# Performance work log

Measured on AMD Instinct MI355X. Metric: run time of the kernel, lower is better.

The kernel has to match this reference:

```python
import jax, jax.numpy as jnp
import numpy as np

N, H = 8192, 256
TOP_K = 16          # k = min(top_k, N-1)
TEMPERATURE = 1.0
NEG_SLOPE = 0.2
NUM_SECTORS = 11


def setup_inputs() -> dict:
    key = jax.random.key(0)
    kE, kW, ka, ks, kA = jax.random.split(key, 5)
    embeddings = jax.random.normal(kE, (N, H), dtype=jnp.float32)
    # xavier-uniform-like scale for W (nn.Linear, bias=False)
    lim = float(np.sqrt(6.0 / (H + H)))
    W = jax.random.uniform(kW, (H, H), dtype=jnp.float32, minval=-lim, maxval=lim)
    # a ~ Normal(0, 1/sqrt(2H))
    a = jax.random.normal(ka, (2 * H,), dtype=jnp.float32) * (1.0 / np.sqrt(2 * H))
    sector_ids = jax.random.randint(ks, (N,), 0, NUM_SECTORS, dtype=jnp.int32)
    active_mask = jax.random.randint(kA, (N,), 0, 2, dtype=jnp.int32).astype(bool)
    return {"embeddings": embeddings, "W": W, "a": a,
            "sector_ids": sector_ids, "active_mask": active_mask}


def reference(embeddings, W, a, sector_ids, active_mask):
    # h = W(embeddings)  (torch Linear: x @ W.T)
    h = embeddings @ W.T                                   # [N, H]
    # attention[i,j] = leaky_relu(a . [h_i, h_j]) = leaky_relu(a1.h_i + a2.h_j)
    # (decomposition of the concat+matmul; same math, avoids O(N^2*2H) tensor)
    a1, a2 = a[:H], a[H:]
    s_i = h @ a1                                           # [N]
    s_j = h @ a2                                           # [N]
    att = jax.nn.leaky_relu(s_i[:, None] + s_j[None, :], NEG_SLOPE) / TEMPERATURE
    # combined mask: active pairs AND same sector
    mask = (active_mask[:, None] & active_mask[None, :]) \
           & (sector_ids[:, None] == sector_ids[None, :])  # [N, N]
    att = jnp.where(mask, att, -jnp.inf)
    k = min(TOP_K, N - 1)
    topk_values, topk_indices = jax.lax.top_k(att, k)      # [N, k] each
    valid = jnp.isfinite(topk_values)                      # invalid = masked-out slots
    # dense padded representation of (edge_index, edge_weight):
    # src = topk_indices, dst = row index, weight = topk_values where valid
    edge_weight = jnp.where(valid, topk_values, 0.0)
    return edge_weight, topk_indices, valid
```

## Files before the change

kernel.cpp:

```cpp
#include <hip/hip_runtime.h>

#define N 8192
#define H 256
#define TOPK 16
#define NSEC 11
#define NEG_SLOPE 0.2
#define NB 256
#define NT 256
#define RPB (N / NB)
#define NSL 8
#define SLICE (N / NSL)
#define IDX_SENT 0x7fffffff

__device__ __forceinline__ bool better(double av, int ai, double bv, int bi) {
    return (av > bv) || (av == bv && ai < bi);
}

__global__ __launch_bounds__(NT) void compute_v_s(
    const float* __restrict__ E, const float* __restrict__ W,
    const float* __restrict__ a,
    float* __restrict__ s1f, double* __restrict__ s2g)
{
    __shared__ float sa[2 * H];
    __shared__ double sv1[H];
    __shared__ double sv2[H];

    int t = threadIdx.x;
    int blk = blockIdx.x;
    int lane = t & 63;
    int w = t >> 6;

    sa[t] = a[t];
    sa[t + H] = a[t + H];
    __syncthreads();

    {
        double a1_0 = 0.0, a1_1 = 0.0, a1_2 = 0.0, a1_3 = 0.0;
        double a2_0 = 0.0, a2_1 = 0.0, a2_2 = 0.0, a2_3 = 0.0;
        for (int j = 0; j < H; j += 4) {
            double w0 = (double)W[(j + 0) * H + t];
            double w1 = (double)W[(j + 1) * H + t];
            double w2 = (double)W[(j + 2) * H + t];
            double w3 = (double)W[(j + 3) * H + t];
            a1_0 += w0 * (double)sa[j + 0];
            a1_1 += w1 * (double)sa[j + 1];
            a1_2 += w2 * (double)sa[j + 2];
            a1_3 += w3 * (double)sa[j + 3];
            a2_0 += w0 * (double)sa[H + j + 0];
            a2_1 += w1 * (double)sa[H + j + 1];
            a2_2 += w2 * (double)sa[H + j + 2];
            a2_3 += w3 * (double)sa[H + j + 3];
        }
        sv1[t] = (a1_0 + a1_1) + (a1_2 + a1_3);
        sv2[t] = (a2_0 + a2_1) + (a2_2 + a2_3);
    }
    __syncthreads();

    {
        float4 e[RPB / 4];
#pragma unroll
        for (int q = 0; q < RPB / 4; ++q) {
            int row = blk * RPB + (w + 4 * q);
            e[q] = ((const float4*)(E + (size_t)row * H))[lane];
        }
        int base = lane * 4;
        double b10 = sv1[base + 0], b11 = sv1[base + 1],
               b12 = sv1[base + 2], b13 = sv1[base + 3];
        double b20 = sv2[base + 0], b21 = sv2[base + 1],
               b22 = sv2[base + 2], b23 = sv2[base + 3];
#pragma unroll
        for (int q = 0; q < RPB / 4; ++q) {
            int row = blk * RPB + (w + 4 * q);
            double acc1 = (double)e[q].x * b10 + (double)e[q].y * b11 +
                          (double)e[q].z * b12 + (double)e[q].w * b13;
            double acc2 = (double)e[q].x * b20 + (double)e[q].y * b21 +
                          (double)e[q].z * b22 + (double)e[q].w * b23;
            for (int o = 32; o > 0; o >>= 1) {
                acc1 += __shfl_down(acc1, o);
                acc2 += __shfl_down(acc2, o);
            }
            if (lane == 0) {
                s1f[row] = (float)acc1;
                s2g[row] = acc2;
            }
        }
    }
}

__global__ __launch_bounds__(NT) void slice_topk(
    const double* __restrict__ s2g, const int* __restrict__ sec,
    const int* __restrict__ act,
    double* __restrict__ candV, int* __restrict__ candI,
    int* __restrict__ cnts)
{
    __shared__ double wV[4][TOPK];
    __shared__ int wI[4][TOPK];
    __shared__ int wCnt[4];

    int bx = blockIdx.x;
    int c = bx >> 3;
    int sl = bx & 7;
    int t = threadIdx.x;
    int lane = t & 63;
    int w = t >> 6;

    int j0 = sl * SLICE + 4 * t;
    int4 a4 = *(const int4*)(act + j0);
    int4 s4 = *(const int4*)(sec + j0);
    double2 d01 = *(const double2*)(s2g + j0);
    double2 d23 = *(const double2*)(s2g + j0 + 2);

    bool p0 = (a4.x != 0) && (s4.x == c);
    bool p1 = (a4.y != 0) && (s4.y == c);
    bool p2 = (a4.z != 0) && (s4.z == c);
    bool p3 = (a4.w != 0) && (s4.w == c);

    double v[4];
    int ix[4];
    v[0] = p0 ? d01.x : -INFINITY;  ix[0] = p0 ? (j0 + 0) : IDX_SENT;
    v[1] = p1 ? d01.y : -INFINITY;  ix[1] = p1 ? (j0 + 1) : IDX_SENT;
    v[2] = p2 ? d23.x : -INFINITY;  ix[2] = p2 ? (j0 + 2) : IDX_SENT;
    v[3] = p3 ? d23.y : -INFINITY;  ix[3] = p3 ? (j0 + 3) : IDX_SENT;

    int cnt = __popcll(__ballot(p0)) + __popcll(__ballot(p1)) +
              __popcll(__ballot(p2)) + __popcll(__ballot(p3));

    for (int r = 0; r < TOPK; ++r) {
        double bv = v[0];
        int bi = ix[0];
#pragma unroll
        for (int p = 1; p < 4; ++p)
            if (better(v[p], ix[p], bv, bi)) { bv = v[p]; bi = ix[p]; }
        for (int o = 32; o > 0; o >>= 1) {
            double ov = __shfl_xor(bv, o);
            int oi = __shfl_xor(bi, o);
            if (better(ov, oi, bv, bi)) { bv = ov; bi = oi; }
        }
#pragma unroll
        for (int p = 0; p < 4; ++p)
            if (ix[p] == bi) { v[p] = -INFINITY; ix[p] = IDX_SENT; }
        if (lane == 0) {
            wV[w][r] = bv;
            wI[w][r] = bi;
        }
    }
    if (lane == 0) wCnt[w] = cnt;
    __syncthreads();

    if (w == 0) {
        double mv = wV[lane >> 4][lane & 15];
        int mi = wI[lane >> 4][lane & 15];
        for (int r = 0; r < TOPK; ++r) {
            double bv = mv;
            int bi = mi;
            for (int o = 32; o > 0; o >>= 1) {
                double ov = __shfl_xor(bv, o);
                int oi = __shfl_xor(bi, o);
                if (better(ov, oi, bv, bi)) { bv = ov; bi = oi; }
            }
            if (mi == bi) { mv = -INFINITY; mi = IDX_SENT; }
            if (lane == 0) {
                candV[bx * TOPK + r] = bv;
                candI[bx * TOPK + r] = bi;
            }
        }
        if (lane == 0) cnts[bx] = wCnt[0] + wCnt[1] + wCnt[2] + wCnt[3];
    }
}

__global__ __launch_bounds__(64) void merge_topk(
    const double* __restrict__ candV, const int* __restrict__ candI,
    const int* __restrict__ cnts, const int* __restrict__ sec,
    const int* __restrict__ act,
    int* __restrict__ top_idx, int* __restrict__ fill_idx,
    int* __restrict__ m_arr)
{
    int c = blockIdx.x;
    int lane = threadIdx.x;

    const double* cbV = candV + (size_t)c * NSL * TOPK;
    const int* cbI = candI + (size_t)c * NSL * TOPK;
    double v0 = cbV[lane];
    int i0 = cbI[lane];
    double v1 = cbV[lane + 64];
    int i1 = cbI[lane + 64];

    for (int r = 0; r < TOPK; ++r) {
        double bv;
        int bi;
        if (better(v0, i0, v1, i1)) { bv = v0; bi = i0; }
        else                        { bv = v1; bi = i1; }
        for (int o = 32; o > 0; o >>= 1) {
            double ov = __shfl_xor(bv, o);
            int oi = __shfl_xor(bi, o);
            if (better(ov, oi, bv, bi)) { bv = ov; bi = oi; }
        }
        if (i0 == bi)      { v0 = -INFINITY; i0 = IDX_SENT; }
        else if (i1 == bi) { v1 = -INFINITY; i1 = IDX_SENT; }
        if (lane == 0) top_idx[c * TOPK + r] = (bi == IDX_SENT) ? -1 : bi;
    }

    int cl = (lane < NSL) ? cnts[c * NSL + lane] : 0;
    for (int o = 32; o > 0; o >>= 1) cl += __shfl_xor(cl, o);
    if (lane == 0) m_arr[c] = (cl < TOPK) ? cl : TOPK;

    int cnt2 = 0;
    for (int basej = 0; basej < N && cnt2 < TOPK; basej += 64) {
        int j = basej + lane;
        bool fail = !((act[j] != 0) && (sec[j] == c));
        unsigned long long mask = __ballot(fail);
        if (fail) {
            int rank = cnt2 + __popcll(mask & ((1ull << lane) - 1));
            if (rank < TOPK) fill_idx[c * TOPK + rank] = j;
        }
        cnt2 += __popcll(mask);
    }
}

__global__ __launch_bounds__(NT) void write_out(const float* __restrict__ s1f,
                                                const double* __restrict__ s2g,
                                                const int* __restrict__ sec,
                                                const int* __restrict__ act,
                                                const int* __restrict__ top_idx,
                                                const int* __restrict__ fill_idx,
                                                const int* __restrict__ m_arr,
                                                float* __restrict__ out) {
    int gid = blockIdx.x * NT + threadIdx.x;
    int i = gid >> 4;
    int slot = gid & 15;

    float wgt = 0.0f;
    float fidx;
    float fvalid = 0.0f;

    if (act[i] == 0) {
        fidx = (float)slot;
    } else {
        int c = sec[i];
        int m = m_arr[c];
        if (slot < m) {
            int j = top_idx[c * TOPK + slot];
            double x = (double)s1f[i] + s2g[j];
            double attv = (x >= 0.0) ? x : NEG_SLOPE * x;
            wgt = (float)attv;
            fvalid = 1.0f;
            fidx = (float)j;
        } else {
            fidx = (float)fill_idx[c * TOPK + (slot - m)];
        }
    }

    out[gid] = wgt;
    out[N * TOPK + gid] = fidx;
    out[2 * N * TOPK + gid] = fvalid;
}

extern "C" void kernel_launch(void* const* d_in, const int* in_sizes, int n_in,
                              void* d_out, int out_size, void* d_ws, size_t ws_size,
                              hipStream_t stream) {
    const float* E = (const float*)d_in[0];
    const float* W = (const float*)d_in[1];
    const float* a = (const float*)d_in[2];
    const int* sec = (const int*)d_in[3];
    const int* act = (const int*)d_in[4];

    char* ws = (char*)d_ws;
    double* s2g = (double*)ws;
    double* candV = s2g + N;
    float* s1f = (float*)(candV + NSEC * NSL * TOPK);
    int* candI = (int*)(s1f + N);
    int* cnts = candI + NSEC * NSL * TOPK;
    int* top_idx = cnts + NSEC * NSL;
    int* fill_idx = top_idx + NSEC * TOPK;
    int* m_arr = fill_idx + NSEC * TOPK;

    float* out = (float*)d_out;

    hipLaunchKernelGGL(compute_v_s, dim3(NB), dim3(NT), 0, stream,
                       E, W, a, s1f, s2g);
    hipLaunchKernelGGL(slice_topk, dim3(NSEC * NSL), dim3(NT), 0, stream,
                       s2g, sec, act, candV, candI, cnts);
    hipLaunchKernelGGL(merge_topk, dim3(NSEC), dim3(64), 0, stream,
                       candV, candI, cnts, sec, act, top_idx, fill_idx, m_arr);
    hipLaunchKernelGGL(write_out, dim3((N * TOPK) / NT), dim3(NT), 0, stream,
                       s1f, s2g, sec, act, top_idx, fill_idx, m_arr, out);
}
```

Baseline: 111.3 us.

## Fuse slice and merge top-k into a single per-sector kernel

Replaces the two-stage top-k (88 slice blocks of 256 threads writing candidates to global memory, then an 11-block merge kernel) with one kernel using 11 blocks of 1024 threads. Each thread handles 8 elements, 16 wavefronts reduce locally, and wave 0 merges 256 candidates from shared memory. Wave 1 computes the fill indices at the same time. This drops a kernel launch and the global round-trip for candidates, but uses far fewer blocks (11) with longer serial per-thread selection loops.

```diff
diff --git a/kernel.cpp b/kernel.cpp
--- a/kernel.cpp
+++ b/kernel.cpp
@@ -8,8 +8,6 @@
 #define NB 256
 #define NT 256
 #define RPB (N / NB)
-#define NSL 8
-#define SLICE (N / NSL)
 #define IDX_SENT 0x7fffffff
 
 __device__ __forceinline__ bool better(double av, int ai, double bv, int bi) {
@@ -87,58 +85,70 @@
     }
 }
 
-__global__ __launch_bounds__(NT) void slice_topk(
+__global__ __launch_bounds__(1024) void sector_topk(
     const double* __restrict__ s2g, const int* __restrict__ sec,
     const int* __restrict__ act,
-    double* __restrict__ candV, int* __restrict__ candI,
-    int* __restrict__ cnts)
+    int* __restrict__ top_idx, int* __restrict__ fill_idx,
+    int* __restrict__ m_arr)
 {
-    __shared__ double wV[4][TOPK];
-    __shared__ int wI[4][TOPK];
-    __shared__ int wCnt[4];
-
-    int bx = blockIdx.x;
-    int c = bx >> 3;
-    int sl = bx & 7;
+    __shared__ double wV[16][TOPK];
+    __shared__ int wI[16][TOPK];
+    __shared__ int wCnt[16];
+
+    int c = blockIdx.x;
     int t = threadIdx.x;
     int lane = t & 63;
     int w = t >> 6;
 
-    int j0 = sl * SLICE + 4 * t;
-    int4 a4 = *(const int4*)(act + j0);
-    int4 s4 = *(const int4*)(sec + j0);
-    double2 d01 = *(const double2*)(s2g + j0);
-    double2 d23 = *(const double2*)(s2g + j0 + 2);
-
-    bool p0 = (a4.x != 0) && (s4.x == c);
-    bool p1 = (a4.y != 0) && (s4.y == c);
-    bool p2 = (a4.z != 0) && (s4.z == c);
-    bool p3 = (a4.w != 0) && (s4.w == c);
-
-    double v[4];
-    int ix[4];
-    v[0] = p0 ? d01.x : -INFINITY;  ix[0] = p0 ? (j0 + 0) : IDX_SENT;
-    v[1] = p1 ? d01.y : -INFINITY;  ix[1] = p1 ? (j0 + 1) : IDX_SENT;
-    v[2] = p2 ? d23.x : -INFINITY;  ix[2] = p2 ? (j0 + 2) : IDX_SENT;
-    v[3] = p3 ? d23.y : -INFINITY;  ix[3] = p3 ? (j0 + 3) : IDX_SENT;
-
-    int cnt = __popcll(__ballot(p0)) + __popcll(__ballot(p1)) +
-              __popcll(__ballot(p2)) + __popcll(__ballot(p3));
+    int j0 = 8 * t;
+    int4 aA = *(const int4*)(act + j0);
+    int4 aB = *(const int4*)(act + j0 + 4);
+    int4 sA = *(const int4*)(sec + j0);
+    int4 sB = *(const int4*)(sec + j0 + 4);
+    double2 d0 = *(const double2*)(s2g + j0);
+    double2 d1 = *(const double2*)(s2g + j0 + 2);
+    double2 d2 = *(const double2*)(s2g + j0 + 4);
+    double2 d3 = *(const double2*)(s2g + j0 + 6);
+
+    bool p[8];
+    p[0] = (aA.x != 0) && (sA.x == c);
+    p[1] = (aA.y != 0) && (sA.y == c);
+    p[2] = (aA.z != 0) && (sA.z == c);
+    p[3] = (aA.w != 0) && (sA.w == c);
+    p[4] = (aB.x != 0) && (sB.x == c);
+    p[5] = (aB.y != 0) && (sB.y == c);
+    p[6] = (aB.z != 0) && (sB.z == c);
+    p[7] = (aB.w != 0) && (sB.w == c);
+
+    double v[8];
+    int ix[8];
+    v[0] = p[0] ? d0.x : -INFINITY;  ix[0] = p[0] ? (j0 + 0) : IDX_SENT;
+    v[1] = p[1] ? d0.y : -INFINITY;  ix[1] = p[1] ? (j0 + 1) : IDX_SENT;
+    v[2] = p[2] ? d1.x : -INFINITY;  ix[2] = p[2] ? (j0 + 2) : IDX_SENT;
+    v[3] = p[3] ? d1.y : -INFINITY;  ix[3] = p[3] ? (j0 + 3) : IDX_SENT;
+    v[4] = p[4] ? d2.x : -INFINITY;  ix[4] = p[4] ? (j0 + 4) : IDX_SENT;
+    v[5] = p[5] ? d2.y : -INFINITY;  ix[5] = p[5] ? (j0 + 5) : IDX_SENT;
+    v[6] = p[6] ? d3.x : -INFINITY;  ix[6] = p[6] ? (j0 + 6) : IDX_SENT;
+    v[7] = p[7] ? d3.y : -INFINITY;  ix[7] = p[7] ? (j0 + 7) : IDX_SENT;
+
+    int cnt = 0;
+#pragma unroll
+    for (int k = 0; k < 8; ++k) cnt += __popcll(__ballot(p[k]));
 
     for (int r = 0; r < TOPK; ++r) {
         double bv = v[0];
         int bi = ix[0];
 #pragma unroll
-        for (int p = 1; p < 4; ++p)
-            if (better(v[p], ix[p], bv, bi)) { bv = v[p]; bi = ix[p]; }
+        for (int q = 1; q < 8; ++q)
+            if (better(v[q], ix[q], bv, bi)) { bv = v[q]; bi = ix[q]; }
         for (int o = 32; o > 0; o >>= 1) {
             double ov = __shfl_xor(bv, o);
             int oi = __shfl_xor(bi, o);
             if (better(ov, oi, bv, bi)) { bv = ov; bi = oi; }
         }
 #pragma unroll
-        for (int p = 0; p < 4; ++p)
-            if (ix[p] == bi) { v[p] = -INFINITY; ix[p] = IDX_SENT; }
+        for (int q = 0; q < 8; ++q)
+            if (ix[q] == bi) { v[q] = -INFINITY; ix[q] = IDX_SENT; }
         if (lane == 0) {
             wV[w][r] = bv;
             wI[w][r] = bi;
@@ -148,72 +158,48 @@
     __syncthreads();
 
     if (w == 0) {
-        double mv = wV[lane >> 4][lane & 15];
-        int mi = wI[lane >> 4][lane & 15];
+        const double* fV = &wV[0][0];
+        const int* fI = &wI[0][0];
+        double mv[4];
+        int mi[4];
+#pragma unroll
+        for (int q = 0; q < 4; ++q) {
+            mv[q] = fV[q * 64 + lane];
+            mi[q] = fI[q * 64 + lane];
+        }
         for (int r = 0; r < TOPK; ++r) {
-            double bv = mv;
-            int bi = mi;
+            double bv = mv[0];
+            int bi = mi[0];
+#pragma unroll
+            for (int q = 1; q < 4; ++q)
+                if (better(mv[q], mi[q], bv, bi)) { bv = mv[q]; bi = mi[q]; }
             for (int o = 32; o > 0; o >>= 1) {
                 double ov = __shfl_xor(bv, o);
                 int oi = __shfl_xor(bi, o);
                 if (better(ov, oi, bv, bi)) { bv = ov; bi = oi; }
             }
-            if (mi == bi) { mv = -INFINITY; mi = IDX_SENT; }
-            if (lane == 0) {
-                candV[bx * TOPK + r] = bv;
-                candI[bx * TOPK + r] = bi;
-            }
-        }
-        if (lane == 0) cnts[bx] = wCnt[0] + wCnt[1] + wCnt[2] + wCnt[3];
-    }
-}
-
-__global__ __launch_bounds__(64) void merge_topk(
-    const double* __restrict__ candV, const int* __restrict__ candI,
-    const int* __restrict__ cnts, const int* __restrict__ sec,
-    const int* __restrict__ act,
-    int* __restrict__ top_idx, int* __restrict__ fill_idx,
-    int* __restrict__ m_arr)
-{
-    int c = blockIdx.x;
-    int lane = threadIdx.x;
-
-    const double* cbV = candV + (size_t)c * NSL * TOPK;
-    const int* cbI = candI + (size_t)c * NSL * TOPK;
-    double v0 = cbV[lane];
-    int i0 = cbI[lane];
-    double v1 = cbV[lane + 64];
-    int i1 = cbI[lane + 64];
-
-    for (int r = 0; r < TOPK; ++r) {
-        double bv;
-        int bi;
-        if (better(v0, i0, v1, i1)) { bv = v0; bi = i0; }
-        else                        { bv = v1; bi = i1; }
-        for (int o = 32; o > 0; o >>= 1) {
-            double ov = __shfl_xor(bv, o);
-            int oi = __shfl_xor(bi, o);
-            if (better(ov, oi, bv, bi)) { bv = ov; bi = oi; }
-        }
-        if (i0 == bi)      { v0 = -INFINITY; i0 = IDX_SENT; }
-        else if (i1 == bi) { v1 = -INFINITY; i1 = IDX_SENT; }
-        if (lane == 0) top_idx[c * TOPK + r] = (bi == IDX_SENT) ? -1 : bi;
-    }
-
-    int cl = (lane < NSL) ? cnts[c * NSL + lane] : 0;
-    for (int o = 32; o > 0; o >>= 1) cl += __shfl_xor(cl, o);
-    if (lane == 0) m_arr[c] = (cl < TOPK) ? cl : TOPK;
-
-    int cnt2 = 0;
-    for (int basej = 0; basej < N && cnt2 < TOPK; basej += 64) {
-        int j = basej + lane;
-        bool fail = !((act[j] != 0) && (sec[j] == c));
-        unsigned long long mask = __ballot(fail);
-        if (fail) {
-            int rank = cnt2 + __popcll(mask & ((1ull << lane) - 1));
-            if (rank < TOPK) fill_idx[c * TOPK + rank] = j;
-        }
-        cnt2 += __popcll(mask);
+#pragma unroll
+            for (int q = 0; q < 4; ++q)
+                if (mi[q] == bi) { mv[q] = -INFINITY; mi[q] = IDX_SENT; }
+            if (lane == 0) top_idx[c * TOPK + r] = (bi == IDX_SENT) ? -1 : bi;
+        }
+        int cl = (lane < 16) ? wCnt[lane] : 0;
+        for (int o = 32; o > 0; o >>= 1) cl += __shfl_xor(cl, o);
+        if (lane == 0) m_arr[c] = (cl < TOPK) ? cl : TOPK;
+    }
+
+    if (w == 1) {
+        int cnt2 = 0;
+        for (int basej = 0; basej < N && cnt2 < TOPK; basej += 64) {
+            int j = basej + lane;
+            bool fail = !((act[j] != 0) && (sec[j] == c));
+            unsigned long long mask = __ballot(fail);
+            if (fail) {
+                int rank = cnt2 + __popcll(mask & ((1ull << lane) - 1));
+                if (rank < TOPK) fill_idx[c * TOPK + rank] = j;
+            }
+            cnt2 += __popcll(mask);
+        }
     }
 }
 
@@ -266,11 +252,8 @@
 
     char* ws = (char*)d_ws;
     double* s2g = (double*)ws;
-    double* candV = s2g + N;
-    float* s1f = (float*)(candV + NSEC * NSL * TOPK);
-    int* candI = (int*)(s1f + N);
-    int* cnts = candI + NSEC * NSL * TOPK;
-    int* top_idx = cnts + NSEC * NSL;
+    float* s1f = (float*)(s2g + N);
+    int* top_idx = (int*)(s1f + N);
     int* fill_idx = top_idx + NSEC * TOPK;
     int* m_arr = fill_idx + NSEC * TOPK;
 
@@ -278,10 +261,8 @@
 
     hipLaunchKernelGGL(compute_v_s, dim3(NB), dim3(NT), 0, stream,
                        E, W, a, s1f, s2g);
-    hipLaunchKernelGGL(slice_topk, dim3(NSEC * NSL), dim3(NT), 0, stream,
-                       s2g, sec, act, candV, candI, cnts);
-    hipLaunchKernelGGL(merge_topk, dim3(NSEC), dim3(64), 0, stream,
-                       candV, candI, cnts, sec, act, top_idx, fill_idx, m_arr);
+    hipLaunchKernelGGL(sector_topk, dim3(NSEC), dim3(1024), 0, stream,
+                       s2g, sec, act, top_idx, fill_idx, m_arr);
     hipLaunchKernelGGL(write_out, dim3((N * TOPK) / NT), dim3(NT), 0, stream,
                        s1f, s2g, sec, act, top_idx, fill_idx, m_arr, out);
 }
```

Result: no change. 111.5 us (+0.2%).
